# Kernel optimization log

Hardware: AMD Instinct MI355X
Metric: run time of the kernel (lower is better)

Reference implementation:

```python
import jax, jax.numpy as jnp
import numpy as np

N1, N2 = 8192, 8192
E1, E2 = 131072, 131072
F_IN, NH, B = 64, 128, 256
D6 = 6 * NH  # set2set in_channels = 768


def _gcn(x, W, b, src, dst, ew, n):
    xw = x @ W
    loop = jnp.arange(n)
    s = jnp.concatenate([src, loop])
    d = jnp.concatenate([dst, loop])
    w = jnp.concatenate([ew, jnp.ones((n,), ew.dtype)])
    deg = jax.ops.segment_sum(w, d, num_segments=n)
    dinv = jnp.where(deg > 0, jax.lax.rsqrt(deg), 0.0)
    norm = (dinv[s] * w * dinv[d])[:, None]
    return jax.ops.segment_sum(xw[s] * norm, d, num_segments=n) + b


def _leaky(x):
    return jax.nn.leaky_relu(x, 0.2)


def _l2norm(x):
    return x / jnp.maximum(jnp.linalg.norm(x, axis=1, keepdims=True), 1e-12)


def _set2set(x, batch, nseg, Wih, Whh, bih, bhh, steps=2):
    # Set2Set pooling: LSTM(input=2d, hidden=d) + segment softmax attention
    d = x.shape[1]
    h = jnp.zeros((nseg, d), x.dtype)
    c = jnp.zeros((nseg, d), x.dtype)
    q_star = jnp.zeros((nseg, 2 * d), x.dtype)
    for _ in range(steps):
        gates = q_star @ Wih.T + h @ Whh.T + bih + bhh
        gi, gf, gg, go = jnp.split(gates, 4, axis=1)  # torch LSTM gate order i,f,g,o
        c = jax.nn.sigmoid(gf) * c + jax.nn.sigmoid(gi) * jnp.tanh(gg)
        h = jax.nn.sigmoid(go) * jnp.tanh(c)
        e = jnp.sum(x * h[batch], axis=1)
        emax = jax.ops.segment_max(e, batch, num_segments=nseg)
        ee = jnp.exp(e - emax[batch])
        a = ee / jax.ops.segment_sum(ee, batch, num_segments=nseg)[batch]
        r = jax.ops.segment_sum(a[:, None] * x, batch, num_segments=nseg)
        q_star = jnp.concatenate([h, r], axis=1)
    return q_star


def setup_inputs():
    key = jax.random.key(0)
    ks = jax.random.split(key, 20)
    f32 = jnp.float32

    def xav(k, shp):
        fan_in, fan_out = shp[-1], shp[0] if len(shp) == 2 else shp[-1]
        lim = float(np.sqrt(6.0 / (shp[0] + shp[1])))
        return jax.random.uniform(k, shp, f32, -lim, lim)

    inp = {}
    inp["features_1"] = jax.random.normal(ks[0], (N1, F_IN), f32)
    inp["features_2"] = jax.random.normal(ks[1], (N2, F_IN), f32)
    inp["edge_attr_1"] = jax.random.uniform(ks[2], (E1,), f32)
    inp["edge_attr_2"] = jax.random.uniform(ks[3], (E2,), f32)
    inp["W0"] = xav(ks[4], (F_IN, NH)); inp["b0"] = jnp.zeros((NH,), f32)
    inp["W1"] = xav(ks[5], (NH, NH)); inp["b1"] = jnp.zeros((NH,), f32)
    inp["W2"] = xav(ks[6], (NH, NH)); inp["b2"] = jnp.zeros((NH,), f32)
    inp["Wih"] = xav(ks[7], (4 * D6, 2 * D6)); inp["bih"] = jnp.zeros((4 * D6,), f32)
    inp["Whh"] = xav(ks[8], (4 * D6, D6)); inp["bhh"] = jnp.zeros((4 * D6,), f32)
    inp["Wp1"] = xav(ks[9], (256, 4 * D6)); inp["bp1"] = jnp.zeros((256,), f32)
    inp["Wp2"] = xav(ks[10], (128, 256)); inp["bp2"] = jnp.zeros((128,), f32)
    inp["Wp3"] = xav(ks[11], (1, 128)); inp["bp3"] = jnp.zeros((1,), f32)
    inp["edge_index_1"] = jax.random.randint(ks[12], (2, E1), 0, N1)
    inp["edge_index_2"] = jax.random.randint(ks[13], (2, E2), 0, N2)
    inp["batch_1"] = jnp.sort(jax.random.randint(ks[14], (N1,), 0, B))
    inp["batch_2"] = jnp.sort(jax.random.randint(ks[15], (N2,), 0, B))
    return inp


def reference(features_1, features_2, edge_attr_1, edge_attr_2,
              W0, b0, W1, b1, W2, b2, Wih, bih, Whh, bhh,
              Wp1, bp1, Wp2, bp2, Wp3, bp3,
              edge_index_1, edge_index_2, batch_1, batch_2):
    s1, d1 = edge_index_1[0], edge_index_1[1]
    s2, d2 = edge_index_2[0], edge_index_2[1]

    f1a = _leaky(_gcn(features_1, W0, b0, s1, d1, edge_attr_1, N1))
    f2a = _leaky(_gcn(features_2, W0, b0, s2, d2, edge_attr_2, N2))
    f1b = _leaky(_gcn(f1a, W1, b1, s1, d1, edge_attr_1, N1))
    f2b = _leaky(_gcn(f2a, W1, b1, s2, d2, edge_attr_2, N2))
    f1c = _leaky(_gcn(f1b, W2, b2, s1, d1, edge_attr_1, N1))
    f2c = _leaky(_gcn(f2b, W2, b2, s2, d2, edge_attr_2, N2))
    h1 = jnp.concatenate([f1a, f1b, f1c], axis=1)  # [N1, 3*NH]
    h2 = jnp.concatenate([f2a, f2b, f2c], axis=1)  # [N2, 3*NH]

    # interaction: cosine-sim map masked to same-graph pairs (len_map)
    ns = _l2norm(h1)
    nv = _l2norm(h2)
    mask = (batch_1[:, None] == batch_2[None, :]).astype(ns.dtype)  # [N1, N2]
    imap = (ns @ nv.T) * mask
    f1 = jnp.concatenate([ns, imap @ nv], axis=1)      # [N1, 6*NH]
    f2 = jnp.concatenate([nv, imap.T @ ns], axis=1)    # [N2, 6*NH]

    g1 = _set2set(f1, batch_1, B, Wih, Whh, bih, bhh)  # [B, 12*NH]
    g2 = _set2set(f2, batch_2, B, Wih, Whh, bih, bhh)  # [B, 12*NH]
    z = jnp.concatenate([g1, g2], axis=1)              # [B, 24*NH]
    z = jax.nn.relu(z @ Wp1.T + bp1)
    z = jax.nn.relu(z @ Wp2.T + bp2)
    z = z @ Wp3.T + bp3
    return jax.nn.sigmoid(z).reshape(-1)
```

## Files before the change

kernel.cpp:

```cpp
#include <hip/hip_runtime.h>
#include <cmath>

#define N_NODES 8192
#define N_EDGES 131072
#define NB      256
#define NH      128
#define D3      384
#define D6      768
#define SMM     96
#define SLD     104

typedef __attribute__((ext_vector_type(8))) short short8v;
typedef __attribute__((ext_vector_type(4))) float f32x4;
typedef unsigned short bf16t;

__device__ __forceinline__ float sigf(float x){ return 1.0f/(1.0f+__expf(-x)); }
__device__ __forceinline__ unsigned short f2bf(float x){
  unsigned u = __float_as_uint(x);
  unsigned r = u + 0x7FFF + ((u>>16)&1);
  return (unsigned short)(r>>16);
}
__device__ __forceinline__ float bfl(unsigned u){ return __uint_as_float(u<<16); }
__device__ __forceinline__ float bfh(unsigned u){ return __uint_as_float(u & 0xFFFF0000u); }
__device__ __forceinline__ float b2f(bf16t u){ return __uint_as_float(((unsigned)u)<<16); }
__device__ __forceinline__ float h0val(const float* bih, const float* bhh, int j){
  float c = sigf(bih[j]+bhh[j]) * tanhf(bih[2*D6+j]+bhh[2*D6+j]);
  return sigf(bih[3*D6+j]+bhh[3*D6+j]) * tanhf(c);
}


__global__ void k_deg(const int* __restrict__ ei1, const float* __restrict__ ea1, float* deg1, int* ecnt1,
                      const int* __restrict__ ei2, const float* __restrict__ ea2, float* deg2, int* ecnt2,
                      const int* __restrict__ b1, const int* __restrict__ b2, int* cnt1, int* cnt2){
  int idx = blockIdx.x*blockDim.x + threadIdx.x;
  int side = idx >= N_EDGES;
  int e = idx & (N_EDGES-1);
  const int* ei = side? ei2:ei1; const float* ea = side? ea2:ea1;
  float* deg = side? deg2:deg1;  int* ecnt = side? ecnt2:ecnt1;
  int d = ei[N_EDGES+e];
  atomicAdd(&deg[d], ea[e]);
  atomicAdd(&ecnt[d], 1);
  if (idx < N_NODES){ atomicAdd(&cnt1[b1[idx]],1); atomicAdd(&cnt2[b2[idx]],1); }
}

__global__ __launch_bounds__(1024) void k_scans(const int* ec1, const int* ec2,
                                                int* off1, int* cur1, int* off2, int* cur2,
                                                const int* c1, const int* c2, int* s1, int* s2){
  __shared__ int ps[1024];
  int bx = blockIdx.x, t = threadIdx.x;
  if (bx < 2){
    const int* cnt = bx? ec2:ec1;
    int* off = bx? off2:off1;
    int* cur = bx? cur2:cur1;
    int base = t*8;
    int loc[8]; int s=0;
    #pragma unroll
    for (int k=0;k<8;k++){ loc[k]=s; s+=cnt[base+k]; }
    ps[t]=s; __syncthreads();
    for (int d=1; d<1024; d<<=1){
      int v = (t>=d)? ps[t-d]:0;
      __syncthreads();
      ps[t]+=v;
      __syncthreads();
    }
    int pre = (t==0)? 0 : ps[t-1];
    #pragma unroll
    for (int k=0;k<8;k++){ int v=pre+loc[k]; off[base+k]=v; cur[base+k]=v; }
    if (t==1023) off[N_NODES]=ps[1023];
  } else {
    const int* c = (bx==3)? c2:c1; int* st = (bx==3)? s2:s1;
    ps[t] = (t<256)? c[t] : 0;
    __syncthreads();
    for (int d=1; d<256; d<<=1){
      int v = (t>=d)? ps[t-d]:0;
      __syncthreads();
      ps[t]+=v;
      __syncthreads();
    }
    if (t<256) st[t+1]=ps[t];
    if (t==0) st[0]=0;
  }
}

__global__ void k_fill(const int* __restrict__ ei1, const float* __restrict__ ea1, const float* __restrict__ d1,
                       int* cur1, int* es1, float* ec1,
                       const int* __restrict__ ei2, const float* __restrict__ ea2, const float* __restrict__ d2,
                       int* cur2, int* es2, float* ec2){
  int idx = blockIdx.x*blockDim.x + threadIdx.x;
  int side = idx >= N_EDGES;
  int e = idx & (N_EDGES-1);
  const int* ei = side? ei2:ei1; const float* ea = side? ea2:ea1;
  const float* deg = side? d2:d1;
  int* cur = side? cur2:cur1; int* es = side? es2:es1; float* ec = side? ec2:ec1;
  int s = ei[e], d = ei[N_EDGES+e];
  int pos = atomicAdd(&cur[d], 1);
  es[pos] = s;
  ec[pos] = rsqrtf(deg[s])*ea[e]*rsqrtf(deg[d]);
}

__global__ __launch_bounds__(256) void k_setup(
    const float* __restrict__ Wih, short* __restrict__ Wih16,
    const float* __restrict__ Wp1, short* __restrict__ Wp116,
    const float* __restrict__ fe1, const float* __restrict__ fe2,
    short* __restrict__ xf1, short* __restrict__ xf2,
    const float* __restrict__ W0, const float* __restrict__ W1, const float* __restrict__ W2,
    bf16t* __restrict__ Wt,
    const float* __restrict__ Whh, const float* __restrict__ bih, const float* __restrict__ bhh,
    float* __restrict__ cvec,
    float* deg1, float* deg2, int* ecnt1, int* ecnt2, int* cnt1, int* cnt2){
  __shared__ float hs[D6];
  int b = blockIdx.x, tid = threadIdx.x;
  if (b < 2304){
    int t = b*256 + tid;
    int n = t/192, q = t - n*192;
    float4 v = ((const float4*)(Wih + (size_t)n*1536 + 768))[q];
    short4 o = { (short)f2bf(v.x), (short)f2bf(v.y), (short)f2bf(v.z), (short)f2bf(v.w) };
    ((short4*)Wih16)[t] = o;
  } else if (b < 3072){
    int t = (b-2304)*256 + tid;
    float4 v = ((const float4*)Wp1)[t];
    short4 o = { (short)f2bf(v.x), (short)f2bf(v.y), (short)f2bf(v.z), (short)f2bf(v.w) };
    ((short4*)Wp116)[t] = o;
  } else if (b < 4096){
    int t = (b-3072)*256 + tid;
    int side = t >= 131072; int i = t & 131071;
    float4 v = ((const float4*)(side? fe2:fe1))[i];
    short4 o = { (short)f2bf(v.x), (short)f2bf(v.y), (short)f2bf(v.z), (short)f2bf(v.w) };
    ((short4*)(side? xf2:xf1))[i] = o;
  } else if (b < 4099){
    int l = b - 4096;
    const float* W = (l==0)? W0 : ((l==1)? W1 : W2);
    int K = (l==0)? 64 : 128;
    bf16t* dst = Wt + ((l==0)? 0 : ((l==1)? 128*64 : 128*64+128*128));
    for (int idx = tid; idx < 128*K; idx += 256){
      int n = idx / K, k = idx - n*K;
      dst[idx] = f2bf(W[k*NH + n]);
    }
  } else if (b < 4867){
    int j0 = (b - 4099)*4;
    for (int k=tid; k<D6; k+=256) hs[k] = h0val(bih,bhh,k);
    __syncthreads();
    int w = tid>>6, lane = tid&63;
    int j = j0 + w;
    const float4* wi = (const float4*)(Wih + (size_t)j*(2*D6));
    const float4* wh = (const float4*)(Whh + (size_t)j*D6);
    const float4* h4 = (const float4*)hs;
    float acc=0;
    #pragma unroll
    for (int m=0;m<3;m++){
      float4 hv = h4[m*64+lane];
      float4 a = wi[m*64+lane];
      float4 bb = wh[m*64+lane];
      acc += hv.x*(a.x+bb.x) + hv.y*(a.y+bb.y) + hv.z*(a.z+bb.z) + hv.w*(a.w+bb.w);
    }
    #pragma unroll
    for (int m=1;m<64;m<<=1) acc += __shfl_xor(acc,m,64);
    if (lane==0) cvec[j]=acc+bih[j]+bhh[j];
  } else {
    int t = (b-4867)*256 + tid;
    if (t < N_NODES){ deg1[t]=1.f; deg2[t]=1.f; ecnt1[t]=0; ecnt2[t]=0; }
    if (t < NB){ cnt1[t]=0; cnt2[t]=0; }
  }
}


__global__ __launch_bounds__(256) void k_xw_mfma(const bf16t* __restrict__ x1, const bf16t* __restrict__ x2,
                                                 int xs, int K, const bf16t* __restrict__ Wt,
                                                 bf16t* __restrict__ xw1, bf16t* __restrict__ xw2){
  int blk = blockIdx.x;
  int side = blk >> 8; int b = blk & 255;
  const bf16t* x = side? x2:x1;
  bf16t* xw = side? xw2:xw1;
  int w = threadIdx.x>>6, lane = threadIdx.x&63;
  int lm = lane&15, quad = lane>>4;
  int r0 = b*32 + (w>>1)*16;
  int c0 = (w&1)*64;
  const bf16t* a = x + (size_t)(r0+lm)*xs + quad*8;
  f32x4 acc[4] = {};
  for (int k=0;k<K;k+=32){
    short8v af = *(const short8v*)(a + k);
    #pragma unroll
    for (int ni=0;ni<4;ni++){
      short8v bf = *(const short8v*)(Wt + (size_t)(c0+ni*16+lm)*K + quad*8 + k);
      acc[ni] = __builtin_amdgcn_mfma_f32_16x16x32_bf16(af, bf, acc[ni], 0,0,0);
    }
  }
  #pragma unroll
  for (int ni=0;ni<4;ni++)
    #pragma unroll
    for (int r=0;r<4;r++){
      int row = r0 + quad*4 + r, col = c0 + ni*16 + lm;
      xw[(size_t)row*NH + col] = f2bf(acc[ni][r]);
    }
}

__global__ __launch_bounds__(256) void k_gather(const bf16t* __restrict__ xw1, const bf16t* __restrict__ xw2,
                                                const int* __restrict__ off1, const int* __restrict__ off2,
                                                const int* __restrict__ es1, const int* __restrict__ es2,
                                                const float* __restrict__ ec1, const float* __restrict__ ec2,
                                                const float* __restrict__ d1, const float* __restrict__ d2,
                                                const float* __restrict__ b,
                                                bf16t* __restrict__ h1, bf16t* __restrict__ h2, int loff,
                                                int l2mode, bf16t* __restrict__ f1, bf16t* __restrict__ f2){
  int blk = blockIdx.x;
  int side = blk >> 10; int bb = blk & 1023;
  const ushort4* xw = (const ushort4*)(side? xw2:xw1);
  const int* off = side? off2:off1;
  const int* es  = side? es2:es1;
  const float* ec= side? ec2:ec1;
  const float* deg = side? d2:d1;
  bf16t* h = side? h2:h1;
  int t = threadIdx.x;
  int i = bb*8 + (t>>5);
  int c4 = t & 31;
  float sc = 1.0f/deg[i];
  ushort4 v = xw[(size_t)i*32 + c4];
  float4 acc = {b2f(v.x)*sc, b2f(v.y)*sc, b2f(v.z)*sc, b2f(v.w)*sc};
  int r = off[i], r1 = off[i+1];
  for (; r+3<r1; r+=4){
    int s0=es[r], s1=es[r+1], s2=es[r+2], s3=es[r+3];
    float w0=ec[r], w1=ec[r+1], w2=ec[r+2], w3=ec[r+3];
    ushort4 u0 = xw[(size_t)s0*32 + c4];
    ushort4 u1 = xw[(size_t)s1*32 + c4];
    ushort4 u2 = xw[(size_t)s2*32 + c4];
    ushort4 u3 = xw[(size_t)s3*32 + c4];
    acc.x += b2f(u0.x)*w0 + b2f(u1.x)*w1 + b2f(u2.x)*w2 + b2f(u3.x)*w3;
    acc.y += b2f(u0.y)*w0 + b2f(u1.y)*w1 + b2f(u2.y)*w2 + b2f(u3.y)*w3;
    acc.z += b2f(u0.z)*w0 + b2f(u1.z)*w1 + b2f(u2.z)*w2 + b2f(u3.z)*w3;
    acc.w += b2f(u0.w)*w0 + b2f(u1.w)*w1 + b2f(u2.w)*w2 + b2f(u3.w)*w3;
  }
  for (; r<r1; r++){
    int s0=es[r]; float w0=ec[r];
    ushort4 u0 = xw[(size_t)s0*32 + c4];
    acc.x+=b2f(u0.x)*w0; acc.y+=b2f(u0.y)*w0; acc.z+=b2f(u0.z)*w0; acc.w+=b2f(u0.w)*w0;
  }
  float4 bv = ((const float4*)b)[c4];
  acc.x+=bv.x; acc.y+=bv.y; acc.z+=bv.z; acc.w+=bv.w;
  acc.x = (acc.x>0.f)?acc.x:0.2f*acc.x;
  acc.y = (acc.y>0.f)?acc.y:0.2f*acc.y;
  acc.z = (acc.z>0.f)?acc.z:0.2f*acc.z;
  acc.w = (acc.w>0.f)?acc.w:0.2f*acc.w;
  if (!l2mode){
    ((ushort4*)(h + (size_t)i*D3 + loff))[c4] =
      make_ushort4(f2bf(acc.x), f2bf(acc.y), f2bf(acc.z), f2bf(acc.w));
  } else {
    ushort4 u0 = ((const ushort4*)(h + (size_t)i*D3))[c4];
    ushort4 u1 = ((const ushort4*)(h + (size_t)i*D3 + 128))[c4];
    float4 v0 = {b2f(u0.x), b2f(u0.y), b2f(u0.z), b2f(u0.w)};
    float4 v1 = {b2f(u1.x), b2f(u1.y), b2f(u1.z), b2f(u1.w)};
    float ss = v0.x*v0.x+v0.y*v0.y+v0.z*v0.z+v0.w*v0.w
             + v1.x*v1.x+v1.y*v1.y+v1.z*v1.z+v1.w*v1.w
             + acc.x*acc.x+acc.y*acc.y+acc.z*acc.z+acc.w*acc.w;
    #pragma unroll
    for (int m=1;m<32;m<<=1) ss += __shfl_xor(ss, m, 64);
    float scale = 1.0f/fmaxf(sqrtf(ss), 1e-12f);
    bf16t* f = side? f2:f1;
    ((ushort4*)(f + (size_t)i*D6))[c4]       = make_ushort4(f2bf(v0.x*scale),f2bf(v0.y*scale),f2bf(v0.z*scale),f2bf(v0.w*scale));
    ((ushort4*)(f + (size_t)i*D6 + 128))[c4] = make_ushort4(f2bf(v1.x*scale),f2bf(v1.y*scale),f2bf(v1.z*scale),f2bf(v1.w*scale));
    ((ushort4*)(f + (size_t)i*D6 + 256))[c4] = make_ushort4(f2bf(acc.x*scale),f2bf(acc.y*scale),f2bf(acc.z*scale),f2bf(acc.w*scale));
  }
}

__global__ __launch_bounds__(256) void k_inter(bf16t* __restrict__ f1, bf16t* __restrict__ f2,
                                               const int* __restrict__ st1, const int* __restrict__ st2,
                                               const float* __restrict__ bih, const float* __restrict__ bhh,
                                               bf16t* __restrict__ Ab){
  __shared__ __align__(16) bf16t Sld[SMM*SLD];
  __shared__ bf16t tbuf[32*392];
  int bx = blockIdx.x;
  int side = bx >> 8, g = bx & (NB-1);
  int i0 = st1[g]; int n1 = st1[g+1]-i0; if (n1>SMM) n1=SMM;
  int j0 = st2[g]; int n2 = st2[g+1]-j0; if (n2>SMM) n2=SMM;
  int cnt = side? n2 : n1;
  int J   = side? n1 : n2;
  int r0base = side? j0 : i0;
  int c0base = side? i0 : j0;
  const bf16t* rowp = (side? f2 : f1);
  const bf16t* colp = (side? f1 : f2);
  const bf16t* src = colp + (size_t)c0base*D6;
  bf16t* dst = (side? f2 : f1) + (size_t)r0base*D6 + D3;
  int t = threadIdx.x, w = t>>6, lane = t&63;
  int lm = lane & 15, quad = lane >> 4;
  {
    uint4* z1 = (uint4*)Sld;
    uint4 zz = make_uint4(0,0,0,0);
    for (int i=t; i<1248; i+=256) z1[i]=zz;
  }
  __syncthreads();
  int nti = (cnt+15)>>4, ntj = (J+15)>>4;
  for (int tile = w; tile < nti*ntj; tile += 4){
    int ti = tile/ntj, tj = tile - ti*ntj;
    int ar = r0base + ti*16 + lm; if (ar > N_NODES-1) ar = N_NODES-1;
    int br = c0base + tj*16 + lm; if (br > N_NODES-1) br = N_NODES-1;
    const bf16t* a = rowp + (size_t)ar*D6 + quad*8;
    const bf16t* b = colp + (size_t)br*D6 + quad*8;
    f32x4 acc = {0,0,0,0};
    #pragma unroll
    for (int k=0; k<384; k+=32){
      short8v af = *(const short8v*)(a + k);
      short8v bf = *(const short8v*)(b + k);
      acc = __builtin_amdgcn_mfma_f32_16x16x32_bf16(af, bf, acc, 0, 0, 0);
    }
    int col = tj*16 + lm;
    #pragma unroll
    for (int r=0;r<4;r++){
      int row = ti*16 + quad*4 + r;
      if (row < cnt && col < J)
        Sld[row*SLD + col] = f2bf(acc[r]);
    }
  }
  __syncthreads();
  for (int r0=0; r0<cnt; r0+=32){
    int mt1 = (cnt - r0 > 16) ? 2 : 1;
    f32x4 acc[2][6] = {};
    for (int kb = 0; kb < J; kb += 32){
      __syncthreads();
      for (int idx = t; idx < 32*48; idx += 256){
        int j = idx/48, cg2 = idx - j*48;
        uint4 v = (kb+j < J)? ((const uint4*)(src + (size_t)(kb+j)*D6))[cg2] : make_uint4(0,0,0,0);
        *(uint4*)(tbuf + j*392 + cg2*8) = v;
      }
      const bf16t* ap = Sld + (r0 + lm)*SLD + kb + quad*8;
      short8v af0 = *(const short8v*)ap;
      short8v af1 = (mt1 > 1)? *(const short8v*)(ap + 16*SLD) : af0;
      __syncthreads();
      #pragma unroll
      for (int ni = 0; ni < 6; ni++){
        int nt = w*6 + ni;
        short8v bf;
        #pragma unroll
        for (int ji = 0; ji < 8; ji++)
          bf[ji] = (short)tbuf[(quad*8 + ji)*392 + nt*16 + lm];
        acc[0][ni] = __builtin_amdgcn_mfma_f32_16x16x32_bf16(af0, bf, acc[0][ni], 0, 0, 0);
        if (mt1 > 1)
          acc[1][ni] = __builtin_amdgcn_mfma_f32_16x16x32_bf16(af1, bf, acc[1][ni], 0, 0, 0);
      }
    }
    for (int mt = 0; mt < mt1; mt++)
      for (int ni = 0; ni < 6; ni++){
        int nt = w*6 + ni;
        #pragma unroll
        for (int r = 0; r < 4; r++){
          int row = r0 + mt*16 + quad*4 + r;
          if (row < cnt) dst[(size_t)row*D6 + nt*16 + lm] = f2bf(acc[mt][ni][r]);
        }
      }
  }
  __syncthreads();
  {
    float4* hs = (float4*)Sld;
    float* e_s = ((float*)Sld) + 768;
    float* part = ((float*)Sld) + 864;
    const bf16t* x = rowp + (size_t)r0base*D6;
    if (t<192){
      int j = t*4;
      hs[t] = make_float4(h0val(bih,bhh,j), h0val(bih,bhh,j+1), h0val(bih,bhh,j+2), h0val(bih,bhh,j+3));
    }
    __syncthreads();
    for (int n=w; n<cnt; n+=4){
      const uint2* xr = (const uint2*)(x + (size_t)n*D6);
      float p = 0;
      #pragma unroll
      for (int m=0;m<3;m++){
        uint2 rv = xr[m*64+lane];
        float4 hvv = hs[m*64+lane];
        p += bfl(rv.x)*hvv.x + bfh(rv.x)*hvv.y + bfl(rv.y)*hvv.z + bfh(rv.y)*hvv.w;
      }
      #pragma unroll
      for (int m=1;m<64;m<<=1) p += __shfl_xor(p,m,64);
      if (lane==0) e_s[n]=p;
    }
    __syncthreads();
    if (w==0){
      float mx=-INFINITY;
      for (int n=lane;n<cnt;n+=64) mx=fmaxf(mx,e_s[n]);
      #pragma unroll
      for (int m=1;m<64;m<<=1) mx=fmaxf(mx,__shfl_xor(mx,m,64));
      float s=0;
      for (int n=lane;n<cnt;n+=64) s+=__expf(e_s[n]-mx);
      #pragma unroll
      for (int m=1;m<64;m<<=1) s+=__shfl_xor(s,m,64);
      float inv=1.0f/s;
      for (int n=lane;n<cnt;n+=64) e_s[n]=__expf(e_s[n]-mx)*inv;
    }
    __syncthreads();
    float av[3][4] = {};
    for (int n=w; n<cnt; n+=4){
      float a = e_s[n];
      const uint2* xr = (const uint2*)(x + (size_t)n*D6);
      #pragma unroll
      for (int m=0;m<3;m++){
        uint2 rv = xr[m*64+lane];
        av[m][0]+=a*bfl(rv.x); av[m][1]+=a*bfh(rv.x); av[m][2]+=a*bfl(rv.y); av[m][3]+=a*bfh(rv.y);
      }
    }
    #pragma unroll
    for (int m=0;m<3;m++)
      *(float4*)&part[w*D6 + (m*64+lane)*4] = make_float4(av[m][0],av[m][1],av[m][2],av[m][3]);
    __syncthreads();
    if (t<192){
      float4 p0 = *(const float4*)&part[0*D6 + t*4];
      float4 p1 = *(const float4*)&part[1*D6 + t*4];
      float4 p2 = *(const float4*)&part[2*D6 + t*4];
      float4 p3 = *(const float4*)&part[3*D6 + t*4];
      float4 s = make_float4(p0.x+p1.x+p2.x+p3.x, p0.y+p1.y+p2.y+p3.y,
                             p0.z+p1.z+p2.z+p3.z, p0.w+p1.w+p2.w+p3.w);
      ushort4 o = make_ushort4(f2bf(s.x), f2bf(s.y), f2bf(s.z), f2bf(s.w));
      ((ushort4*)(Ab + (size_t)(side*NB+g)*D6))[t]=o;
    }
  }
}


__global__ __launch_bounds__(256) void k_att(const bf16t* __restrict__ f1, const bf16t* __restrict__ f2,
                                             const float* __restrict__ hbase, int perseg,
                                             const float* __restrict__ bih, const float* __restrict__ bhh,
                                             const int* __restrict__ st1, const int* __restrict__ st2,
                                             bf16t* __restrict__ dst16, long sidestep, long dstride){
  __shared__ float4 hs[192];
  __shared__ float e_s[SMM];
  __shared__ float part[4][D6];
  int side = blockIdx.x >> 8, g = blockIdx.x & (NB-1);
  const int* st = side? st2:st1;
  int n0 = st[g]; int cnt = st[g+1]-n0; if (cnt>SMM) cnt=SMM;
  const bf16t* x = (side? f2:f1) + (size_t)n0*D6;
  int t = threadIdx.x, w = t>>6, lane = t&63;
  if (t<192){
    if (perseg){
      hs[t] = ((const float4*)(hbase + (size_t)(side*NB+g)*D6))[t];
    } else {
      int j = t*4;
      hs[t] = make_float4(h0val(bih,bhh,j), h0val(bih,bhh,j+1), h0val(bih,bhh,j+2), h0val(bih,bhh,j+3));
    }
  }
  __syncthreads();
  for (int n=w; n<cnt; n+=4){
    const uint2* xr = (const uint2*)(x + (size_t)n*D6);
    float p = 0;
    #pragma unroll
    for (int m=0;m<3;m++){
      uint2 rv = xr[m*64+lane];
      float4 hvv = hs[m*64+lane];
      p += bfl(rv.x)*hvv.x + bfh(rv.x)*hvv.y + bfl(rv.y)*hvv.z + bfh(rv.y)*hvv.w;
    }
    #pragma unroll
    for (int m=1;m<64;m<<=1) p += __shfl_xor(p,m,64);
    if (lane==0) e_s[n]=p;
  }
  __syncthreads();
  if (w==0){
    float mx=-INFINITY;
    for (int n=lane;n<cnt;n+=64) mx=fmaxf(mx,e_s[n]);
    #pragma unroll
    for (int m=1;m<64;m<<=1) mx=fmaxf(mx,__shfl_xor(mx,m,64));
    float s=0;
    for (int n=lane;n<cnt;n+=64) s+=__expf(e_s[n]-mx);
    #pragma unroll
    for (int m=1;m<64;m<<=1) s+=__shfl_xor(s,m,64);
    float inv=1.0f/s;
    for (int n=lane;n<cnt;n+=64) e_s[n]=__expf(e_s[n]-mx)*inv;
  }
  __syncthreads();
  float av[3][4] = {};
  for (int n=w; n<cnt; n+=4){
    float a = e_s[n];
    const uint2* xr = (const uint2*)(x + (size_t)n*D6);
    #pragma unroll
    for (int m=0;m<3;m++){
      uint2 rv = xr[m*64+lane];
      av[m][0]+=a*bfl(rv.x); av[m][1]+=a*bfh(rv.x); av[m][2]+=a*bfl(rv.y); av[m][3]+=a*bfh(rv.y);
    }
  }
  #pragma unroll
  for (int m=0;m<3;m++)
    *(float4*)&part[w][(m*64+lane)*4] = make_float4(av[m][0],av[m][1],av[m][2],av[m][3]);
  __syncthreads();
  if (t<192){
    float4 p0 = *(const float4*)&part[0][t*4];
    float4 p1 = *(const float4*)&part[1][t*4];
    float4 p2 = *(const float4*)&part[2][t*4];
    float4 p3 = *(const float4*)&part[3][t*4];
    float4 s = make_float4(p0.x+p1.x+p2.x+p3.x, p0.y+p1.y+p2.y+p3.y,
                           p0.z+p1.z+p2.z+p3.z, p0.w+p1.w+p2.w+p3.w);
    ushort4 o = make_ushort4(f2bf(s.x), f2bf(s.y), f2bf(s.z), f2bf(s.w));
    ushort4* dp = (ushort4*)(dst16 + side*sidestep + (size_t)g*dstride);
    dp[t]=o;
  }
}

__global__ __launch_bounds__(256) void k_gates(const short* __restrict__ A16,
                                               const short* __restrict__ B16,
                                               const float* __restrict__ cvec,
                                               const float* __restrict__ bih, const float* __restrict__ bhh,
                                               float* __restrict__ h1s, bf16t* __restrict__ z16){
  __shared__ float gbuf[4][16][66];
  int w = threadIdx.x >> 6, lane = threadIdx.x & 63;
  int lm = lane & 15, quad = lane >> 4;
  int bm = blockIdx.x * 16;
  int jb = blockIdx.y * 64;
  const short* a = A16 + (size_t)(bm + lm)*768 + quad*8;
  const short* b = B16 + (size_t)(w*768 + jb + lm)*768 + quad*8;
  f32x4 acc0={0,0,0,0}, acc1={0,0,0,0}, acc2={0,0,0,0}, acc3={0,0,0,0};
  for (int k=0; k<768; k+=32){
    short8v af = *(const short8v*)(a + k);
    short8v b0 = *(const short8v*)(b + k);
    short8v b1 = *(const short8v*)(b + 16*768 + k);
    short8v b2 = *(const short8v*)(b + 32*768 + k);
    short8v b3 = *(const short8v*)(b + 48*768 + k);
    acc0 = __builtin_amdgcn_mfma_f32_16x16x32_bf16(af, b0, acc0, 0, 0, 0);
    acc1 = __builtin_amdgcn_mfma_f32_16x16x32_bf16(af, b1, acc1, 0, 0, 0);
    acc2 = __builtin_amdgcn_mfma_f32_16x16x32_bf16(af, b2, acc2, 0, 0, 0);
    acc3 = __builtin_amdgcn_mfma_f32_16x16x32_bf16(af, b3, acc3, 0, 0, 0);
  }
  #pragma unroll
  for (int r=0;r<4;r++){
    gbuf[w][quad*4+r][lm]      = acc0[r];
    gbuf[w][quad*4+r][16+lm]   = acc1[r];
    gbuf[w][quad*4+r][32+lm]   = acc2[r];
    gbuf[w][quad*4+r][48+lm]   = acc3[r];
  }
  __syncthreads();
  int t = threadIdx.x;
  #pragma unroll
  for (int u=0; u<4; u++){
    int p = t + u*256;
    int mm = p>>6, jj = p&63;
    int j = jb + jj, m = bm + mm;
    float g4[4];
    #pragma unroll
    for (int q=0;q<4;q++) g4[q] = gbuf[q][mm][jj] + cvec[q*D6 + j];
    float c0j = sigf(bih[j]+bhh[j]) * tanhf(bih[2*D6+j]+bhh[2*D6+j]);
    float c = sigf(g4[1])*c0j + sigf(g4[0])*tanhf(g4[2]);
    float h = sigf(g4[3])*tanhf(c);
    h1s[(size_t)m*D6 + j] = h;
    int side = m>>8, g = m&255;
    z16[(size_t)g*3072 + side*1536 + j] = f2bf(h);
  }
}

__global__ __launch_bounds__(256) void k_gemm_mfma_p1(const short* __restrict__ A16,
                                                      const short* __restrict__ B16,
                                                      float* __restrict__ pout){
  int w = threadIdx.x >> 6, lane = threadIdx.x & 63;
  int lm = lane & 15, quad = lane >> 4;
  int bm = blockIdx.x * 16;
  int bn = w * 64;
  int kbase = blockIdx.y * 192;
  const short* a = A16 + (size_t)(bm + lm)*3072 + quad*8 + kbase;
  const short* b = B16 + (size_t)(bn + lm)*3072 + quad*8 + kbase;
  f32x4 acc0={0,0,0,0}, acc1={0,0,0,0}, acc2={0,0,0,0}, acc3={0,0,0,0};
  for (int k=0; k<192; k+=32){
    short8v af = *(const short8v*)(a + k);
    short8v b0 = *(const short8v*)(b + k);
    short8v b1 = *(const short8v*)(b + 16*3072 + k);
    short8v b2 = *(const short8v*)(b + 32*3072 + k);
    short8v b3 = *(const short8v*)(b + 48*3072 + k);
    acc0 = __builtin_amdgcn_mfma_f32_16x16x32_bf16(af, b0, acc0, 0, 0, 0);
    acc1 = __builtin_amdgcn_mfma_f32_16x16x32_bf16(af, b1, acc1, 0, 0, 0);
    acc2 = __builtin_amdgcn_mfma_f32_16x16x32_bf16(af, b2, acc2, 0, 0, 0);
    acc3 = __builtin_amdgcn_mfma_f32_16x16x32_bf16(af, b3, acc3, 0, 0, 0);
  }
  float* po = pout + (size_t)blockIdx.y*256*256;
  #pragma unroll
  for (int r=0;r<4;r++){
    size_t base = (size_t)(bm + quad*4 + r)*256 + bn + lm;
    po[base]      = acc0[r];
    po[base + 16] = acc1[r];
    po[base + 32] = acc2[r];
    po[base + 48] = acc3[r];
  }
}

__global__ __launch_bounds__(128) void k_p23(const float* __restrict__ pbuf, const float* __restrict__ bp1,
                                             const float* __restrict__ Wp2, const float* __restrict__ bp2,
                                             const float* __restrict__ Wp3, const float* __restrict__ bp3,
                                             float* __restrict__ out){
  __shared__ float zr[256];
  __shared__ float ws[2];
  int m = blockIdx.x, t = threadIdx.x;
  float2 zacc = ((const float2*)(bp1))[t];
  #pragma unroll
  for (int p=0;p<16;p++){
    float2 v = ((const float2*)(pbuf + (size_t)p*256*256 + (size_t)m*256))[t];
    zacc.x += v.x; zacc.y += v.y;
  }
  zr[2*t]   = fmaxf(zacc.x, 0.f);
  zr[2*t+1] = fmaxf(zacc.y, 0.f);
  __syncthreads();
  const float4* wrow = (const float4*)(Wp2 + (size_t)t*256);
  const float4* z4 = (const float4*)zr;
  float acc = bp2[t];
  #pragma unroll 8
  for (int k=0;k<64;k++){
    float4 wv = wrow[k], zv = z4[k];
    acc += wv.x*zv.x + wv.y*zv.y + wv.z*zv.z + wv.w*zv.w;
  }
  float p = fmaxf(acc,0.f)*Wp3[t];
  #pragma unroll
  for (int o=32;o;o>>=1) p += __shfl_down(p,o,64);
  if ((t&63)==0) ws[t>>6]=p;
  __syncthreads();
  if (t==0){ float v=ws[0]+ws[1]+bp3[0]; out[m]=1.0f/(1.0f+__expf(-v)); }
}


extern "C" void kernel_launch(void* const* d_in, const int* in_sizes, int n_in,
                              void* d_out, int out_size, void* d_ws, size_t ws_size,
                              hipStream_t stream){
  const float* feat1=(const float*)d_in[0];
  const float* feat2=(const float*)d_in[1];
  const float* ea1  =(const float*)d_in[2];
  const float* ea2  =(const float*)d_in[3];
  const float* W0=(const float*)d_in[4];  const float* b0=(const float*)d_in[5];
  const float* W1=(const float*)d_in[6];  const float* b1=(const float*)d_in[7];
  const float* W2=(const float*)d_in[8];  const float* b2=(const float*)d_in[9];
  const float* Wih=(const float*)d_in[10]; const float* bih=(const float*)d_in[11];
  const float* Whh=(const float*)d_in[12]; const float* bhh=(const float*)d_in[13];
  const float* Wp1=(const float*)d_in[14]; const float* bp1=(const float*)d_in[15];
  const float* Wp2=(const float*)d_in[16]; const float* bp2=(const float*)d_in[17];
  const float* Wp3=(const float*)d_in[18]; const float* bp3=(const float*)d_in[19];
  const int* ei1=(const int*)d_in[20]; const int* ei2=(const int*)d_in[21];
  const int* batch1=(const int*)d_in[22]; const int* batch2=(const int*)d_in[23];
  float* out = (float*)d_out;

  float* base = (float*)d_ws;
  size_t off = 0;
  auto alloc = [&](size_t n)->float* { float* r = base + off; off += (n + 255) & ~(size_t)255; return r; };
  float* deg1 = alloc(N_NODES);          float* deg2 = alloc(N_NODES);
  bf16t* xw1  = (bf16t*)alloc((size_t)N_NODES*NH/2);
  bf16t* xw2  = (bf16t*)alloc((size_t)N_NODES*NH/2);
  bf16t* hb1  = (bf16t*)alloc((size_t)N_NODES*D3/2);
  bf16t* hb2  = (bf16t*)alloc((size_t)N_NODES*D3/2);
  bf16t* xf1  = (bf16t*)alloc((size_t)N_NODES*64/2);
  bf16t* xf2  = (bf16t*)alloc((size_t)N_NODES*64/2);
  bf16t* Wtb  = (bf16t*)alloc((size_t)(128*64 + 2*128*128)/2);
  bf16t* f1   = (bf16t*)alloc((size_t)N_NODES*D6/2);
  bf16t* f2   = (bf16t*)alloc((size_t)N_NODES*D6/2);
  float* ecoef1 = alloc(N_EDGES);        float* ecoef2 = alloc(N_EDGES);
  float* cvec = alloc(4*D6);
  float* h1s  = alloc((size_t)512*D6);
  bf16t* zbuf16 = (bf16t*)alloc((size_t)256*3072/2);
  float* pbuf = alloc((size_t)16*256*256);
  short* Abuf16 = (short*)alloc((size_t)512*D6/2);
  short* Wih16  = (short*)alloc((size_t)3072*D6/2);
  short* Wp116  = (short*)alloc((size_t)256*3072/2);
  int* cnt1 = (int*)alloc(NB);   int* cnt2 = (int*)alloc(NB);
  int* st1  = (int*)alloc(NB+1); int* st2  = (int*)alloc(NB+1);
  int* ecnt1= (int*)alloc(N_NODES); int* ecnt2 = (int*)alloc(N_NODES);
  int* eoff1= (int*)alloc(N_NODES+1); int* eoff2 = (int*)alloc(N_NODES+1);
  int* ecur1= (int*)alloc(N_NODES); int* ecur2 = (int*)alloc(N_NODES);
  int* esrc1= (int*)alloc(N_EDGES); int* esrc2 = (int*)alloc(N_EDGES);
  (void)ws_size; (void)in_sizes; (void)n_in; (void)out_size;

  k_setup  <<<4899,256,0,stream>>>(Wih,Wih16, Wp1,Wp116, feat1,feat2,(short*)xf1,(short*)xf2,
                                   W0,W1,W2,Wtb, Whh,bih,bhh, cvec,
                                   deg1,deg2,ecnt1,ecnt2,cnt1,cnt2);
  k_deg    <<<1024,256,0,stream>>>(ei1,ea1,deg1,ecnt1, ei2,ea2,deg2,ecnt2, batch1,batch2,cnt1,cnt2);
  k_scans  <<<4,1024,0,stream>>>(ecnt1,ecnt2,eoff1,ecur1,eoff2,ecur2, cnt1,cnt2,st1,st2);
  k_fill   <<<1024,256,0,stream>>>(ei1,ea1,deg1,ecur1,esrc1,ecoef1, ei2,ea2,deg2,ecur2,esrc2,ecoef2);

  const float* bs[3]={b0,b1,b2};
  const bf16t* Wts[3]={Wtb, Wtb+128*64, Wtb+128*64+128*128};
  for (int l=0;l<3;l++){
    const bf16t* x1 = (l==0)? xf1 : (hb1 + (l-1)*NH);
    const bf16t* x2 = (l==0)? xf2 : (hb2 + (l-1)*NH);
    int xs = (l==0)? 64 : D3;
    int K  = (l==0)? 64 : NH;
    k_xw_mfma<<<512,256,0,stream>>>(x1,x2,xs,K,Wts[l],xw1,xw2);
    k_gather <<<2048,256,0,stream>>>(xw1,xw2,eoff1,eoff2,esrc1,esrc2,ecoef1,ecoef2,
                                     deg1,deg2,bs[l],hb1,hb2,l*NH,(l==2)?1:0,f1,f2);
  }

  k_inter <<<512,256,0,stream>>>(f1,f2,st1,st2,bih,bhh,(bf16t*)Abuf16);

  k_gates<<<dim3(32,12),256,0,stream>>>(Abuf16, Wih16, cvec, bih, bhh, h1s, zbuf16);

  k_att<<<512,256,0,stream>>>(f1,f2,h1s,1,bih,bhh,st1,st2,
                              zbuf16+768,(long)1536,(long)3072);

  k_gemm_mfma_p1<<<dim3(16,16),256,0,stream>>>((const short*)zbuf16, Wp116, pbuf);
  k_p23 <<<256,128,0,stream>>>(pbuf, bp1, Wp2, bp2, Wp3, bp3, out);
}
```

Before: 349.9 us.

## Fuse GCN gather with next layer's XW GEMM and fuse MLP head kernels

Adds a k_gxw kernel that does the edge gather, bias and leaky-ReLU for 16 rows per block, then immediately computes those rows times the next layer's weights with MFMA. This removes two separate XW launches and ping-pongs between two xw buffers. The MLP head is also folded into one kernel (k_mlp) that runs the full K=3072 GEMM per 16-row block and applies layers 2 and 3 in place, dropping the split-K partial buffer and the second launch. The trade-off is that k_mlp launches only 16 blocks with a long serial K loop, which may leave the GPU underused, and the gather stage has half as many blocks.

```diff
diff --git a/kernel.cpp b/kernel.cpp
--- a/kernel.cpp
+++ b/kernel.cpp
@@ -194,6 +194,83 @@
     }
 }
 
+__global__ __launch_bounds__(256) void k_gxw(
+    const bf16t* __restrict__ xwi1, const bf16t* __restrict__ xwi2,
+    const int* __restrict__ off1, const int* __restrict__ off2,
+    const int* __restrict__ es1, const int* __restrict__ es2,
+    const float* __restrict__ ec1, const float* __restrict__ ec2,
+    const float* __restrict__ d1, const float* __restrict__ d2,
+    const float* __restrict__ bias, int loff,
+    bf16t* __restrict__ h1, bf16t* __restrict__ h2,
+    const bf16t* __restrict__ Wl,
+    bf16t* __restrict__ xwo1, bf16t* __restrict__ xwo2){
+  int blk = blockIdx.x;
+  int side = blk >> 9; int b = blk & 511;
+  const ushort4* xw = (const ushort4*)(side? xwi2:xwi1);
+  const int* off = side? off2:off1;
+  const int* es  = side? es2:es1;
+  const float* ec= side? ec2:ec1;
+  const float* deg = side? d2:d1;
+  bf16t* h = side? h2:h1;
+  int t = threadIdx.x;
+  int c4 = t & 31;
+  float4 bv = ((const float4*)bias)[c4];
+  #pragma unroll
+  for (int grp=0; grp<2; grp++){
+    int i = b*16 + grp*8 + (t>>5);
+    float sc = 1.0f/deg[i];
+    ushort4 v = xw[(size_t)i*32 + c4];
+    float4 acc = {b2f(v.x)*sc, b2f(v.y)*sc, b2f(v.z)*sc, b2f(v.w)*sc};
+    int r = off[i], r1 = off[i+1];
+    for (; r+3<r1; r+=4){
+      int s0=es[r], s1=es[r+1], s2=es[r+2], s3=es[r+3];
+      float w0=ec[r], w1=ec[r+1], w2=ec[r+2], w3=ec[r+3];
+      ushort4 u0 = xw[(size_t)s0*32 + c4];
+      ushort4 u1 = xw[(size_t)s1*32 + c4];
+      ushort4 u2 = xw[(size_t)s2*32 + c4];
+      ushort4 u3 = xw[(size_t)s3*32 + c4];
+      acc.x += b2f(u0.x)*w0 + b2f(u1.x)*w1 + b2f(u2.x)*w2 + b2f(u3.x)*w3;
+      acc.y += b2f(u0.y)*w0 + b2f(u1.y)*w1 + b2f(u2.y)*w2 + b2f(u3.y)*w3;
+      acc.z += b2f(u0.z)*w0 + b2f(u1.z)*w1 + b2f(u2.z)*w2 + b2f(u3.z)*w3;
+      acc.w += b2f(u0.w)*w0 + b2f(u1.w)*w1 + b2f(u2.w)*w2 + b2f(u3.w)*w3;
+    }
+    for (; r<r1; r++){
+      int s0=es[r]; float w0=ec[r];
+      ushort4 u0 = xw[(size_t)s0*32 + c4];
+      acc.x+=b2f(u0.x)*w0; acc.y+=b2f(u0.y)*w0; acc.z+=b2f(u0.z)*w0; acc.w+=b2f(u0.w)*w0;
+    }
+    acc.x+=bv.x; acc.y+=bv.y; acc.z+=bv.z; acc.w+=bv.w;
+    acc.x = (acc.x>0.f)?acc.x:0.2f*acc.x;
+    acc.y = (acc.y>0.f)?acc.y:0.2f*acc.y;
+    acc.z = (acc.z>0.f)?acc.z:0.2f*acc.z;
+    acc.w = (acc.w>0.f)?acc.w:0.2f*acc.w;
+    ((ushort4*)(h + (size_t)i*D3 + loff))[c4] =
+      make_ushort4(f2bf(acc.x), f2bf(acc.y), f2bf(acc.z), f2bf(acc.w));
+  }
+  __syncthreads();
+  int w = t>>6, lane = t&63;
+  int lm = lane&15, quad = lane>>4;
+  const bf16t* x = (side? h2:h1) + loff;
+  int r0 = b*16;
+  int c0 = w*32;
+  const bf16t* a = x + (size_t)(r0+lm)*D3 + quad*8;
+  bf16t* xwo = side? xwo2:xwo1;
+  f32x4 acc0={0,0,0,0}, acc1={0,0,0,0};
+  for (int k=0;k<128;k+=32){
+    short8v af = *(const short8v*)(a + k);
+    short8v b0 = *(const short8v*)(Wl + (size_t)(c0+lm)*128 + quad*8 + k);
+    short8v b1 = *(const short8v*)(Wl + (size_t)(c0+16+lm)*128 + quad*8 + k);
+    acc0 = __builtin_amdgcn_mfma_f32_16x16x32_bf16(af, b0, acc0, 0,0,0);
+    acc1 = __builtin_amdgcn_mfma_f32_16x16x32_bf16(af, b1, acc1, 0,0,0);
+  }
+  #pragma unroll
+  for (int r=0;r<4;r++){
+    int row = r0 + quad*4 + r;
+    xwo[(size_t)row*NH + c0 + lm]      = f2bf(acc0[r]);
+    xwo[(size_t)row*NH + c0 + 16 + lm] = f2bf(acc1[r]);
+  }
+}
+
 __global__ __launch_bounds__(256) void k_gather(const bf16t* __restrict__ xw1, const bf16t* __restrict__ xw2,
                                                 const int* __restrict__ off1, const int* __restrict__ off2,
                                                 const int* __restrict__ es1, const int* __restrict__ es2,
@@ -538,18 +615,22 @@
   }
 }
 
-__global__ __launch_bounds__(256) void k_gemm_mfma_p1(const short* __restrict__ A16,
-                                                      const short* __restrict__ B16,
-                                                      float* __restrict__ pout){
-  int w = threadIdx.x >> 6, lane = threadIdx.x & 63;
-  int lm = lane & 15, quad = lane >> 4;
-  int bm = blockIdx.x * 16;
-  int bn = w * 64;
-  int kbase = blockIdx.y * 192;
-  const short* a = A16 + (size_t)(bm + lm)*3072 + quad*8 + kbase;
-  const short* b = B16 + (size_t)(bn + lm)*3072 + quad*8 + kbase;
+__global__ __launch_bounds__(256) void k_mlp(const short* __restrict__ A16,
+                                             const short* __restrict__ B16,
+                                             const float* __restrict__ bp1,
+                                             const float* __restrict__ Wp2, const float* __restrict__ bp2,
+                                             const float* __restrict__ Wp3, const float* __restrict__ bp3,
+                                             float* __restrict__ out){
+  __shared__ float zr[16][264];
+  __shared__ float ws2[2][2];
+  int t = threadIdx.x;
+  int w = t>>6, lane = t&63;
+  int lm = lane&15, quad = lane>>4;
+  int bm = blockIdx.x*16;
+  const short* a = A16 + (size_t)(bm + lm)*3072 + quad*8;
+  const short* b = B16 + (size_t)(w*64 + lm)*3072 + quad*8;
   f32x4 acc0={0,0,0,0}, acc1={0,0,0,0}, acc2={0,0,0,0}, acc3={0,0,0,0};
-  for (int k=0; k<192; k+=32){
+  for (int k=0; k<3072; k+=32){
     short8v af = *(const short8v*)(a + k);
     short8v b0 = *(const short8v*)(b + k);
     short8v b1 = *(const short8v*)(b + 16*3072 + k);
@@ -560,47 +641,36 @@
     acc2 = __builtin_amdgcn_mfma_f32_16x16x32_bf16(af, b2, acc2, 0, 0, 0);
     acc3 = __builtin_amdgcn_mfma_f32_16x16x32_bf16(af, b3, acc3, 0, 0, 0);
   }
-  float* po = pout + (size_t)blockIdx.y*256*256;
+  int bn = w*64;
   #pragma unroll
   for (int r=0;r<4;r++){
-    size_t base = (size_t)(bm + quad*4 + r)*256 + bn + lm;
-    po[base]      = acc0[r];
-    po[base + 16] = acc1[r];
-    po[base + 32] = acc2[r];
-    po[base + 48] = acc3[r];
-  }
-}
-
-__global__ __launch_bounds__(128) void k_p23(const float* __restrict__ pbuf, const float* __restrict__ bp1,
-                                             const float* __restrict__ Wp2, const float* __restrict__ bp2,
-                                             const float* __restrict__ Wp3, const float* __restrict__ bp3,
-                                             float* __restrict__ out){
-  __shared__ float zr[256];
-  __shared__ float ws[2];
-  int m = blockIdx.x, t = threadIdx.x;
-  float2 zacc = ((const float2*)(bp1))[t];
-  #pragma unroll
-  for (int p=0;p<16;p++){
-    float2 v = ((const float2*)(pbuf + (size_t)p*256*256 + (size_t)m*256))[t];
-    zacc.x += v.x; zacc.y += v.y;
-  }
-  zr[2*t]   = fmaxf(zacc.x, 0.f);
-  zr[2*t+1] = fmaxf(zacc.y, 0.f);
-  __syncthreads();
-  const float4* wrow = (const float4*)(Wp2 + (size_t)t*256);
-  const float4* z4 = (const float4*)zr;
-  float acc = bp2[t];
-  #pragma unroll 8
-  for (int k=0;k<64;k++){
-    float4 wv = wrow[k], zv = z4[k];
-    acc += wv.x*zv.x + wv.y*zv.y + wv.z*zv.z + wv.w*zv.w;
-  }
-  float p = fmaxf(acc,0.f)*Wp3[t];
-  #pragma unroll
-  for (int o=32;o;o>>=1) p += __shfl_down(p,o,64);
-  if ((t&63)==0) ws[t>>6]=p;
-  __syncthreads();
-  if (t==0){ float v=ws[0]+ws[1]+bp3[0]; out[m]=1.0f/(1.0f+__expf(-v)); }
+    int row = quad*4+r;
+    zr[row][bn+lm]      = fmaxf(acc0[r] + bp1[bn+lm], 0.f);
+    zr[row][bn+16+lm]   = fmaxf(acc1[r] + bp1[bn+16+lm], 0.f);
+    zr[row][bn+32+lm]   = fmaxf(acc2[r] + bp1[bn+32+lm], 0.f);
+    zr[row][bn+48+lm]   = fmaxf(acc3[r] + bp1[bn+48+lm], 0.f);
+  }
+  __syncthreads();
+  for (int pair=0; pair<8; pair++){
+    int row = pair*2 + (t>>7);
+    int tt = t & 127;
+    const float4* wrow = (const float4*)(Wp2 + (size_t)tt*256);
+    const float4* z4 = (const float4*)&zr[row][0];
+    float acc = bp2[tt];
+    #pragma unroll 8
+    for (int k=0;k<64;k++){
+      float4 wv = wrow[k], zv = z4[k];
+      acc += wv.x*zv.x + wv.y*zv.y + wv.z*zv.z + wv.w*zv.w;
+    }
+    float p = fmaxf(acc,0.f)*Wp3[tt];
+    #pragma unroll
+    for (int o=32;o;o>>=1) p += __shfl_down(p,o,64);
+    if (lane==0) ws2[w>>1][w&1] = p;
+    __syncthreads();
+    if (t==0)   out[bm+pair*2]   = 1.0f/(1.0f+__expf(-(ws2[0][0]+ws2[0][1]+bp3[0])));
+    if (t==128) out[bm+pair*2+1] = 1.0f/(1.0f+__expf(-(ws2[1][0]+ws2[1][1]+bp3[0])));
+    __syncthreads();
+  }
 }
 
 
@@ -627,8 +697,10 @@
   size_t off = 0;
   auto alloc = [&](size_t n)->float* { float* r = base + off; off += (n + 255) & ~(size_t)255; return r; };
   float* deg1 = alloc(N_NODES);          float* deg2 = alloc(N_NODES);
-  bf16t* xw1  = (bf16t*)alloc((size_t)N_NODES*NH/2);
-  bf16t* xw2  = (bf16t*)alloc((size_t)N_NODES*NH/2);
+  bf16t* xwA1 = (bf16t*)alloc((size_t)N_NODES*NH/2);
+  bf16t* xwA2 = (bf16t*)alloc((size_t)N_NODES*NH/2);
+  bf16t* xwB1 = (bf16t*)alloc((size_t)N_NODES*NH/2);
+  bf16t* xwB2 = (bf16t*)alloc((size_t)N_NODES*NH/2);
   bf16t* hb1  = (bf16t*)alloc((size_t)N_NODES*D3/2);
   bf16t* hb2  = (bf16t*)alloc((size_t)N_NODES*D3/2);
   bf16t* xf1  = (bf16t*)alloc((size_t)N_NODES*64/2);
@@ -640,7 +712,6 @@
   float* cvec = alloc(4*D6);
   float* h1s  = alloc((size_t)512*D6);
   bf16t* zbuf16 = (bf16t*)alloc((size_t)256*3072/2);
-  float* pbuf = alloc((size_t)16*256*256);
   short* Abuf16 = (short*)alloc((size_t)512*D6/2);
   short* Wih16  = (short*)alloc((size_t)3072*D6/2);
   short* Wp116  = (short*)alloc((size_t)256*3072/2);
@@ -659,17 +730,15 @@
   k_scans  <<<4,1024,0,stream>>>(ecnt1,ecnt2,eoff1,ecur1,eoff2,ecur2, cnt1,cnt2,st1,st2);
   k_fill   <<<1024,256,0,stream>>>(ei1,ea1,deg1,ecur1,esrc1,ecoef1, ei2,ea2,deg2,ecur2,esrc2,ecoef2);
 
-  const float* bs[3]={b0,b1,b2};
-  const bf16t* Wts[3]={Wtb, Wtb+128*64, Wtb+128*64+128*128};
-  for (int l=0;l<3;l++){
-    const bf16t* x1 = (l==0)? xf1 : (hb1 + (l-1)*NH);
-    const bf16t* x2 = (l==0)? xf2 : (hb2 + (l-1)*NH);
-    int xs = (l==0)? 64 : D3;
-    int K  = (l==0)? 64 : NH;
-    k_xw_mfma<<<512,256,0,stream>>>(x1,x2,xs,K,Wts[l],xw1,xw2);
-    k_gather <<<2048,256,0,stream>>>(xw1,xw2,eoff1,eoff2,esrc1,esrc2,ecoef1,ecoef2,
-                                     deg1,deg2,bs[l],hb1,hb2,l*NH,(l==2)?1:0,f1,f2);
-  }
+  const bf16t* Wt1 = Wtb + 128*64;
+  const bf16t* Wt2 = Wtb + 128*64 + 128*128;
+  k_xw_mfma<<<512,256,0,stream>>>(xf1,xf2,64,64,Wtb,xwA1,xwA2);
+  k_gxw<<<1024,256,0,stream>>>(xwA1,xwA2, eoff1,eoff2, esrc1,esrc2, ecoef1,ecoef2,
+                               deg1,deg2, b0, 0, hb1,hb2, Wt1, xwB1,xwB2);
+  k_gxw<<<1024,256,0,stream>>>(xwB1,xwB2, eoff1,eoff2, esrc1,esrc2, ecoef1,ecoef2,
+                               deg1,deg2, b1, NH, hb1,hb2, Wt2, xwA1,xwA2);
+  k_gather <<<2048,256,0,stream>>>(xwA1,xwA2,eoff1,eoff2,esrc1,esrc2,ecoef1,ecoef2,
+                                   deg1,deg2,b2,hb1,hb2,2*NH,1,f1,f2);
 
   k_inter <<<512,256,0,stream>>>(f1,f2,st1,st2,bih,bhh,(bf16t*)Abuf16);
 
@@ -678,6 +747,5 @@
   k_att<<<512,256,0,stream>>>(f1,f2,h1s,1,bih,bhh,st1,st2,
                               zbuf16+768,(long)1536,(long)3072);
 
-  k_gemm_mfma_p1<<<dim3(16,16),256,0,stream>>>((const short*)zbuf16, Wp116, pbuf);
-  k_p23 <<<256,128,0,stream>>>(pbuf, bp1, Wp2, bp2, Wp3, bp3, out);
-}
+  k_mlp <<<16,256,0,stream>>>((const short*)zbuf16, Wp116, bp1, Wp2, bp2, Wp3, bp3, out);
+}
```

Result: slower. 447.6 us (+27.9%).
